# Performance work log

Hardware: AMD Instinct MI355X
Metric: run time of the kernel (lower is better)

Reference implementation:

```python
import jax, jax.numpy as jnp
import numpy as np

INPUT_SIZE = 4
HIDDEN = 2048
OUTPUT_SIZE = 2
NOISE_STD = 0.05
ALPHA = 0.2
RANK = 2
N_SUPPORTS = 2
GDIM = 2 * RANK + INPUT_SIZE  # gaussian_basis_dim default
BATCH = 32
SEQ = 1000


def setup_inputs() -> dict:
    key = jax.random.key(0)
    ks = jax.random.split(key, 8)
    inp = jax.random.normal(ks[0], (BATCH, SEQ, INPUT_SIZE), dtype=jnp.float32)
    noise = jax.random.normal(ks[1], (BATCH, SEQ, HIDDEN), dtype=jnp.float32)
    gaussian_basis = jax.random.normal(ks[2], (GDIM, HIDDEN), dtype=jnp.float32)
    # supports: block indicator masks over hidden units (equal split, weights=None)
    sup = np.zeros((N_SUPPORTS, HIDDEN), dtype=np.float32)
    l = HIDDEN // N_SUPPORTS
    for i in range(N_SUPPORTS):
        sup[i, l * i:l * (i + 1)] = 1.0
    supports = jnp.asarray(sup)
    wi_weights = jax.random.normal(ks[3], (INPUT_SIZE, N_SUPPORTS, GDIM), dtype=jnp.float32)
    m_weights = jax.random.normal(ks[4], (RANK, N_SUPPORTS, GDIM), dtype=jnp.float32) / jnp.sqrt(jnp.float32(HIDDEN))
    n_weights = jax.random.normal(ks[5], (RANK, N_SUPPORTS, GDIM), dtype=jnp.float32) / jnp.sqrt(jnp.float32(HIDDEN))
    wo_weights = jax.random.normal(ks[6], (OUTPUT_SIZE, N_SUPPORTS, GDIM), dtype=jnp.float32) / jnp.float32(HIDDEN)
    wi_biases = jnp.zeros((INPUT_SIZE, N_SUPPORTS), dtype=jnp.float32)
    m_biases = jnp.zeros((RANK, N_SUPPORTS), dtype=jnp.float32)
    n_biases = jnp.zeros((RANK, N_SUPPORTS), dtype=jnp.float32)
    h0_weights = jnp.zeros((N_SUPPORTS, GDIM), dtype=jnp.float32)
    return {
        "input": inp, "noise": noise,
        "wi_weights": wi_weights, "m_weights": m_weights, "n_weights": n_weights,
        "wo_weights": wo_weights, "wi_biases": wi_biases, "m_biases": m_biases,
        "n_biases": n_biases, "h0_weights": h0_weights,
        "gaussian_basis": gaussian_basis, "supports": supports,
    }


def _proxy_params(wi_weights, m_weights, n_weights, wo_weights,
                  wi_biases, m_biases, n_biases, h0_weights,
                  gaussian_basis, supports):
    # (X, S, G) @ (G, H) -> (X, S, H); mask by supports (S, H); sum over S
    def mix(w):
        return jnp.einsum('xsg,gh->xsh', w, gaussian_basis)
    wi = jnp.sum(mix(wi_weights) * supports, axis=1) + wi_biases @ supports      # (I, H)
    m = (jnp.sum(mix(m_weights) * supports, axis=1) + m_biases @ supports).T     # (H, R)
    n = (jnp.sum(mix(n_weights) * supports, axis=1) + n_biases @ supports).T     # (H, R)
    wo = jnp.sum(mix(wo_weights) * supports, axis=1).T                            # (H, O)
    h0 = jnp.sum((h0_weights @ gaussian_basis) * supports, axis=0)                # (H,)
    return wi, m, n, wo, h0


def reference(input, noise, wi_weights, m_weights, n_weights, wo_weights,
              wi_biases, m_biases, n_biases, h0_weights, gaussian_basis, supports):
    wi, m, n, wo, h0 = _proxy_params(wi_weights, m_weights, n_weights, wo_weights,
                                     wi_biases, m_biases, n_biases, h0_weights,
                                     gaussian_basis, supports)
    B = input.shape[0]
    # Precompute external input projection for all steps: (B, T, H)
    xin = jnp.einsum('bti,ih->bth', input, wi)
    h_init = jnp.broadcast_to(h0, (B, h0.shape[0]))
    r_init = jnp.tanh(h_init)

    noise_T = jnp.swapaxes(noise, 0, 1)  # (T, B, H)
    xin_T = jnp.swapaxes(xin, 0, 1)      # (T, B, H)

    def step(carry, xs):
        h, r = carry
        noise_t, xin_t = xs
        h = h + NOISE_STD * noise_t + ALPHA * (-h + (r @ n) @ m.T + xin_t)
        r = jnp.tanh(h)
        return (h, r), r

    _, rs = jax.lax.scan(step, (h_init, r_init), (noise_T, xin_T))  # rs: (T, B, H)
    output = jnp.einsum('tbh,ho->bto', rs, wo)  # (B, T, O)
    return output
```

## Files before the change

### kernel.cpp

```cpp
#include <hip/hip_runtime.h>

#define BATCH 32
#define SEQT 1000
#define INSZ 4
#define HID 2048
#define NOISE_STD 0.05f
#define ALPHA 0.2f
#define ONE_M_ALPHA (1.0f - ALPHA)

#define NTHREADS 512
#define NWAVES 8
#define EPT 4
#define PF 4

typedef float v2f __attribute__((ext_vector_type(2)));

__device__ __forceinline__ v2f pk_fma(v2f a, v2f b, v2f c) {
    v2f d; asm("v_pk_fma_f32 %0, %1, %2, %3" : "=v"(d) : "v"(a), "v"(b), "v"(c)); return d;
}
__device__ __forceinline__ v2f pk_mul(v2f a, v2f b) {
    v2f d; asm("v_pk_mul_f32 %0, %1, %2" : "=v"(d) : "v"(a), "v"(b)); return d;
}
__device__ __forceinline__ v2f pk_add(v2f a, v2f b) {
    v2f d; asm("v_pk_add_f32 %0, %1, %2" : "=v"(d) : "v"(a), "v"(b)); return d;
}
#define C2(v) (v2f{(v), (v)})


__device__ __forceinline__ void tree64_pair(float& a, float& b) {
    asm("s_nop 1\n\t"
        "v_add_f32_dpp %0, %0, %0 row_shr:1 row_mask:0xf bank_mask:0xf bound_ctrl:0\n\t"
        "v_add_f32_dpp %1, %1, %1 row_shr:1 row_mask:0xf bank_mask:0xf bound_ctrl:0\n\t"
        "v_add_f32_dpp %0, %0, %0 row_shr:2 row_mask:0xf bank_mask:0xf bound_ctrl:0\n\t"
        "v_add_f32_dpp %1, %1, %1 row_shr:2 row_mask:0xf bank_mask:0xf bound_ctrl:0\n\t"
        "v_add_f32_dpp %0, %0, %0 row_shr:4 row_mask:0xf bank_mask:0xf bound_ctrl:0\n\t"
        "v_add_f32_dpp %1, %1, %1 row_shr:4 row_mask:0xf bank_mask:0xf bound_ctrl:0\n\t"
        "v_add_f32_dpp %0, %0, %0 row_shr:8 row_mask:0xf bank_mask:0xf bound_ctrl:0\n\t"
        "v_add_f32_dpp %1, %1, %1 row_shr:8 row_mask:0xf bank_mask:0xf bound_ctrl:0\n\t"
        "v_add_f32_dpp %0, %0, %0 row_bcast:15 row_mask:0xf bank_mask:0xf bound_ctrl:0\n\t"
        "v_add_f32_dpp %1, %1, %1 row_bcast:15 row_mask:0xf bank_mask:0xf bound_ctrl:0\n\t"
        "v_add_f32_dpp %0, %0, %0 row_bcast:31 row_mask:0xf bank_mask:0xf bound_ctrl:0\n\t"
        "v_add_f32_dpp %1, %1, %1 row_bcast:31 row_mask:0xf bank_mask:0xf bound_ctrl:0"
        : "+v"(a), "+v"(b));
}

__device__ __forceinline__ void bfly8_pair(float& a, float& b) {
    asm("s_nop 1\n\t"
        "v_add_f32_dpp %0, %0, %0 quad_perm:[1,0,3,2] row_mask:0xf bank_mask:0xf\n\t"
        "v_add_f32_dpp %1, %1, %1 quad_perm:[1,0,3,2] row_mask:0xf bank_mask:0xf\n\t"
        "v_add_f32_dpp %0, %0, %0 quad_perm:[2,3,0,1] row_mask:0xf bank_mask:0xf\n\t"
        "v_add_f32_dpp %1, %1, %1 quad_perm:[2,3,0,1] row_mask:0xf bank_mask:0xf\n\t"
        "v_add_f32_dpp %0, %0, %0 row_half_mirror row_mask:0xf bank_mask:0xf\n\t"
        "v_add_f32_dpp %1, %1, %1 row_half_mirror row_mask:0xf bank_mask:0xf"
        : "+v"(a), "+v"(b));
}

__device__ __forceinline__ v2f pade_tanh(v2f x) {
    const v2f x2  = pk_mul(x, x);
    const v2f num = pk_mul(x, pk_fma(x2, pk_add(x2, C2(105.0f)), C2(945.0f)));
    const v2f den = pk_fma(x2, pk_fma(x2, C2(15.0f), C2(420.0f)), C2(945.0f));
    v2f r;
    r.x = num.x * __builtin_amdgcn_rcpf(den.x);
    r.y = num.y * __builtin_amdgcn_rcpf(den.y);
    r.x = fminf(fmaxf(r.x, -1.0f), 1.0f);
    r.y = fminf(fmaxf(r.y, -1.0f), 1.0f);
    return r;
}

__device__ __forceinline__ float pade_tanh_s(float x) {
    const float x2 = x * x;
    const float num = x * fmaf(x2, x2 + 105.0f, 945.0f);
    const float den = fmaf(x2, fmaf(x2, 15.0f, 420.0f), 945.0f);
    float r = num * __builtin_amdgcn_rcpf(den);
    return fminf(fmaxf(r, -1.0f), 1.0f);
}

#define LDS_BARRIER() __asm__ volatile("s_waitcnt lgkmcnt(0)\ns_barrier" ::: "memory")

__global__ __launch_bounds__(NTHREADS)
void rnn_kernel(const float* __restrict__ input,
                const float* __restrict__ noise,
                const float* __restrict__ wi_w,
                const float* __restrict__ m_w,
                const float* __restrict__ n_w,
                const float* __restrict__ wo_w,
                const float* __restrict__ wi_b,
                const float* __restrict__ m_b,
                const float* __restrict__ n_b,
                const float* __restrict__ h0_w,
                const float* __restrict__ gb,
                const float* __restrict__ sup,
                float* __restrict__ out)
{
    __shared__ __align__(16) float2 sDup[SEQT][4];
    __shared__ float2 sW[2][NWAVES][65];
    __shared__ float2 sO[2][NWAVES][65];

    const int b    = blockIdx.x;
    const int tid  = threadIdx.x;
    const int wave = tid >> 6;
    const int lane = tid & 63;

    const float4* inRow4 = reinterpret_cast<const float4*>(input + (size_t)b * SEQT * INSZ);
    for (int i = tid; i < SEQT; i += NTHREADS) {
        const float4 v = inRow4[i];
        sDup[i][0] = make_float2(v.x, v.x);
        sDup[i][1] = make_float2(v.y, v.y);
        sDup[i][2] = make_float2(v.z, v.z);
        sDup[i][3] = make_float2(v.w, v.w);
    }

    v2f wiA[INSZ][2];
    v2f mA0v[2], mA1v[2], n0v[2], n1v[2], wo0v[2], wo1v[2], hv[2];
    v2f q0 = {0.f, 0.f}, q1 = q0, q2 = q0, q3 = q0;

    #pragma unroll
    for (int e = 0; e < EPT; ++e) {
        const int h = tid * 4 + e;
        const int pi = e >> 1, pc = e & 1;
        float gv[8];
        #pragma unroll
        for (int g = 0; g < 8; ++g) gv[g] = gb[g * HID + h];
        const float s0 = sup[h];
        const float s1 = sup[HID + h];

        auto mix = [&](const float* w) -> float {
            float a0 = 0.f, a1 = 0.f;
            #pragma unroll
            for (int g = 0; g < 8; ++g) { a0 += w[g] * gv[g]; a1 += w[8 + g] * gv[g]; }
            return s0 * a0 + s1 * a1;
        };

        #pragma unroll
        for (int i = 0; i < INSZ; ++i)
            wiA[i][pi][pc] = ALPHA * (mix(wi_w + i * 16) + wi_b[i * 2 + 0] * s0 + wi_b[i * 2 + 1] * s1);
        mA0v[pi][pc] = ALPHA * (mix(m_w)      + m_b[0] * s0 + m_b[1] * s1);
        mA1v[pi][pc] = ALPHA * (mix(m_w + 16) + m_b[2] * s0 + m_b[3] * s1);
        const float n0 = mix(n_w)      + n_b[0] * s0 + n_b[1] * s1;
        const float n1 = mix(n_w + 16) + n_b[2] * s0 + n_b[3] * s1;
        const float w0 = mix(wo_w);
        const float w1 = mix(wo_w + 16);
        n0v[pi][pc] = n0;  n1v[pi][pc] = n1;
        wo0v[pi][pc] = w0; wo1v[pi][pc] = w1;
        {
            float a0 = 0.f, a1 = 0.f;
            #pragma unroll
            for (int g = 0; g < 8; ++g) { a0 += h0_w[g] * gv[g]; a1 += h0_w[8 + g] * gv[g]; }
            const float h0v = s0 * a0 + s1 * a1;
            hv[pi][pc] = h0v;
            const float r = pade_tanh_s(h0v);
            q0[pc] += r * n0;  q1[pc] += r * n1;
            q2[pc] += r * w0;  q3[pc] += r * w1;
        }
    }

    const float4* nP4 = reinterpret_cast<const float4*>(noise + (size_t)b * SEQT * HID);
    const int rowStride = HID / 4;
    float4 nb0 = nP4[0 * rowStride + tid];
    float4 nb1 = nP4[1 * rowStride + tid];
    float4 nb2 = nP4[2 * rowStride + tid];
    float4 nb3 = nP4[3 * rowStride + tid];

    float* outRow = out + (size_t)b * SEQT * 2;

    __syncthreads();
    const float4* dRow = reinterpret_cast<const float4*>(sDup);
    float4 ivA0 = dRow[0], ivB0 = dRow[1];
    float4 ivA1 = dRow[2], ivB1 = dRow[3];
    float4 ivA2 = dRow[4], ivB2 = dRow[5];
    float4 ivA3 = dRow[6], ivB3 = dRow[7];

    const v2f cNS  = C2(NOISE_STD);
    const v2f cOMA = C2(ONE_M_ALPHA);

    auto do_step = [&](int t, int PAR, float4& nbuf, float4& ivAreg, float4& ivBreg) {
        float w0 = q0.x + q0.y;
        float w1 = q1.x + q1.y;
        tree64_pair(w0, w1);
        sW[PAR][wave][lane] = make_float2(w0, w1);

        LDS_BARRIER();

        const float2 prw = sW[PAR][lane & 7][63];
        const float2 pro = sO[PAR ^ 1][lane & 7][63];

        float oz = q2.x + q2.y;
        float ow = q3.x + q3.y;
        tree64_pair(oz, ow);
        sO[PAR][wave][lane] = make_float2(oz, ow);

        const int tpre = (t + PF < SEQT) ? (t + PF) : (SEQT - 1);
        const float4 nv4 = nbuf;
        nbuf = nP4[(size_t)tpre * rowStride + tid];
        const float4 ivA = ivAreg, ivB = ivBreg;
        ivAreg = dRow[2 * tpre];
        ivBreg = dRow[2 * tpre + 1];

        const v2f nlo = {nv4.x, nv4.y}, nhi = {nv4.z, nv4.w};
        const v2f ix = {ivA.x, ivA.y}, iy = {ivA.z, ivA.w};
        const v2f iz = {ivB.x, ivB.y}, iw = {ivB.z, ivB.w};
        v2f acc0 = pk_mul(wiA[0][0], ix);
        v2f acc1 = pk_mul(wiA[0][1], ix);
        acc0 = pk_fma(wiA[1][0], iy, acc0);  acc1 = pk_fma(wiA[1][1], iy, acc1);
        acc0 = pk_fma(wiA[2][0], iz, acc0);  acc1 = pk_fma(wiA[2][1], iz, acc1);
        acc0 = pk_fma(wiA[3][0], iw, acc0);  acc1 = pk_fma(wiA[3][1], iw, acc1);
        acc0 = pk_fma(nlo, cNS, acc0);       acc1 = pk_fma(nhi, cNS, acc1);
        acc0 = pk_fma(hv[0], cOMA, acc0);    acc1 = pk_fma(hv[1], cOMA, acc1);

        float y0 = prw.x, y1 = prw.y;
        bfly8_pair(y0, y1);

        float o0 = pro.x, o1 = pro.y;
        bfly8_pair(o0, o1);
        if (t >= 2 && tid == ((t & 7) << 6))
            *reinterpret_cast<float2*>(outRow + (t - 2) * 2) = make_float2(o0, o1);

        const v2f y0p = {y0, y0}, y1p = {y1, y1};
        v2f h2a = pk_fma(mA1v[0], y1p, acc0);
        v2f h2b = pk_fma(mA1v[1], y1p, acc1);
        h2a = pk_fma(mA0v[0], y0p, h2a);
        h2b = pk_fma(mA0v[1], y0p, h2b);
        hv[0] = h2a; hv[1] = h2b;
        const v2f r2a = pade_tanh(h2a);
        const v2f r2b = pade_tanh(h2b);
        q0 = pk_fma(r2b, n0v[1],  pk_mul(r2a, n0v[0]));
        q1 = pk_fma(r2b, n1v[1],  pk_mul(r2a, n1v[0]));
        q2 = pk_fma(r2b, wo0v[1], pk_mul(r2a, wo0v[0]));
        q3 = pk_fma(r2b, wo1v[1], pk_mul(r2a, wo1v[0]));
    };

    for (int t = 0; t < SEQT; t += PF) {
        do_step(t,     0, nb0, ivA0, ivB0);
        do_step(t + 1, 1, nb1, ivA1, ivB1);
        do_step(t + 2, 0, nb2, ivA2, ivB2);
        do_step(t + 3, 1, nb3, ivA3, ivB3);
    }

    {
        float a9 = q2.x + q2.y;
        float b9 = q3.x + q3.y;
        tree64_pair(a9, b9);
        sW[0][wave][lane] = make_float2(a9, b9);
        LDS_BARRIER();
        const float2 pr9 = sW[0][lane & 7][63];
        const float2 pr8 = sO[1][lane & 7][63];
        float x9 = pr9.x, y9 = pr9.y;
        float x8 = pr8.x, y8 = pr8.y;
        bfly8_pair(x9, y9);
        bfly8_pair(x8, y8);
        if (tid == 0) {
            *reinterpret_cast<float2*>(outRow + 998 * 2) = make_float2(x8, y8);
            *reinterpret_cast<float2*>(outRow + 999 * 2) = make_float2(x9, y9);
        }
    }
}

extern "C" void kernel_launch(void* const* d_in, const int* in_sizes, int n_in,
                              void* d_out, int out_size, void* d_ws, size_t ws_size,
                              hipStream_t stream) {
    const float* input = (const float*)d_in[0];
    const float* noise = (const float*)d_in[1];
    const float* wi_w  = (const float*)d_in[2];
    const float* m_w   = (const float*)d_in[3];
    const float* n_w   = (const float*)d_in[4];
    const float* wo_w  = (const float*)d_in[5];
    const float* wi_b  = (const float*)d_in[6];
    const float* m_b   = (const float*)d_in[7];
    const float* n_b   = (const float*)d_in[8];
    const float* h0_w  = (const float*)d_in[9];
    const float* gb    = (const float*)d_in[10];
    const float* sup   = (const float*)d_in[11];
    float* out = (float*)d_out;

    rnn_kernel<<<dim3(BATCH), dim3(NTHREADS), 0, stream>>>(
        input, noise, wi_w, m_w, n_w, wo_w, wi_b, m_b, n_b, h0_w, gb, sup, out);
}
```

Measured before the change: 830.4 us.

## Halve block to 4 waves with 8 elements per thread and merge reductions

Shrinks each block from 512 to 256 threads, so each thread owns 8 hidden units and the cross-wave exchange covers 4 waves instead of 8. The recurrence reduction and the output reduction are merged into one four-value DPP tree and one float4 LDS slot, removing the separate output exchange array. This cuts barrier cost and the per-step cross-wave combine latency on the serial critical path. In exchange each thread does twice the per-step elementwise work and needs more registers.

```diff
diff --git a/kernel.cpp b/kernel.cpp
--- a/kernel.cpp
+++ b/kernel.cpp
@@ -8,9 +8,10 @@
 #define ALPHA 0.2f
 #define ONE_M_ALPHA (1.0f - ALPHA)
 
-#define NTHREADS 512
-#define NWAVES 8
-#define EPT 4
+#define NTHREADS 256
+#define NWAVES 4
+#define EPT 8
+#define NPAIR 4
 #define PF 4
 
 typedef float v2f __attribute__((ext_vector_type(2)));
@@ -26,6 +27,34 @@
 }
 #define C2(v) (v2f{(v), (v)})
 
+__device__ __forceinline__ void tree64_quad(float& a, float& b, float& c, float& d) {
+    asm("s_nop 1\n\t"
+        "v_add_f32_dpp %0, %0, %0 row_shr:1 row_mask:0xf bank_mask:0xf bound_ctrl:0\n\t"
+        "v_add_f32_dpp %1, %1, %1 row_shr:1 row_mask:0xf bank_mask:0xf bound_ctrl:0\n\t"
+        "v_add_f32_dpp %2, %2, %2 row_shr:1 row_mask:0xf bank_mask:0xf bound_ctrl:0\n\t"
+        "v_add_f32_dpp %3, %3, %3 row_shr:1 row_mask:0xf bank_mask:0xf bound_ctrl:0\n\t"
+        "v_add_f32_dpp %0, %0, %0 row_shr:2 row_mask:0xf bank_mask:0xf bound_ctrl:0\n\t"
+        "v_add_f32_dpp %1, %1, %1 row_shr:2 row_mask:0xf bank_mask:0xf bound_ctrl:0\n\t"
+        "v_add_f32_dpp %2, %2, %2 row_shr:2 row_mask:0xf bank_mask:0xf bound_ctrl:0\n\t"
+        "v_add_f32_dpp %3, %3, %3 row_shr:2 row_mask:0xf bank_mask:0xf bound_ctrl:0\n\t"
+        "v_add_f32_dpp %0, %0, %0 row_shr:4 row_mask:0xf bank_mask:0xf bound_ctrl:0\n\t"
+        "v_add_f32_dpp %1, %1, %1 row_shr:4 row_mask:0xf bank_mask:0xf bound_ctrl:0\n\t"
+        "v_add_f32_dpp %2, %2, %2 row_shr:4 row_mask:0xf bank_mask:0xf bound_ctrl:0\n\t"
+        "v_add_f32_dpp %3, %3, %3 row_shr:4 row_mask:0xf bank_mask:0xf bound_ctrl:0\n\t"
+        "v_add_f32_dpp %0, %0, %0 row_shr:8 row_mask:0xf bank_mask:0xf bound_ctrl:0\n\t"
+        "v_add_f32_dpp %1, %1, %1 row_shr:8 row_mask:0xf bank_mask:0xf bound_ctrl:0\n\t"
+        "v_add_f32_dpp %2, %2, %2 row_shr:8 row_mask:0xf bank_mask:0xf bound_ctrl:0\n\t"
+        "v_add_f32_dpp %3, %3, %3 row_shr:8 row_mask:0xf bank_mask:0xf bound_ctrl:0\n\t"
+        "v_add_f32_dpp %0, %0, %0 row_bcast:15 row_mask:0xf bank_mask:0xf bound_ctrl:0\n\t"
+        "v_add_f32_dpp %1, %1, %1 row_bcast:15 row_mask:0xf bank_mask:0xf bound_ctrl:0\n\t"
+        "v_add_f32_dpp %2, %2, %2 row_bcast:15 row_mask:0xf bank_mask:0xf bound_ctrl:0\n\t"
+        "v_add_f32_dpp %3, %3, %3 row_bcast:15 row_mask:0xf bank_mask:0xf bound_ctrl:0\n\t"
+        "v_add_f32_dpp %0, %0, %0 row_bcast:31 row_mask:0xf bank_mask:0xf bound_ctrl:0\n\t"
+        "v_add_f32_dpp %1, %1, %1 row_bcast:31 row_mask:0xf bank_mask:0xf bound_ctrl:0\n\t"
+        "v_add_f32_dpp %2, %2, %2 row_bcast:31 row_mask:0xf bank_mask:0xf bound_ctrl:0\n\t"
+        "v_add_f32_dpp %3, %3, %3 row_bcast:31 row_mask:0xf bank_mask:0xf bound_ctrl:0"
+        : "+v"(a), "+v"(b), "+v"(c), "+v"(d));
+}
 
 __device__ __forceinline__ void tree64_pair(float& a, float& b) {
     asm("s_nop 1\n\t"
@@ -44,14 +73,25 @@
         : "+v"(a), "+v"(b));
 }
 
-__device__ __forceinline__ void bfly8_pair(float& a, float& b) {
+__device__ __forceinline__ void bfly4_quad(float& a, float& b, float& c, float& d) {
+    asm("s_nop 1\n\t"
+        "v_add_f32_dpp %0, %0, %0 quad_perm:[1,0,3,2] row_mask:0xf bank_mask:0xf\n\t"
+        "v_add_f32_dpp %1, %1, %1 quad_perm:[1,0,3,2] row_mask:0xf bank_mask:0xf\n\t"
+        "v_add_f32_dpp %2, %2, %2 quad_perm:[1,0,3,2] row_mask:0xf bank_mask:0xf\n\t"
+        "v_add_f32_dpp %3, %3, %3 quad_perm:[1,0,3,2] row_mask:0xf bank_mask:0xf\n\t"
+        "v_add_f32_dpp %0, %0, %0 quad_perm:[2,3,0,1] row_mask:0xf bank_mask:0xf\n\t"
+        "v_add_f32_dpp %1, %1, %1 quad_perm:[2,3,0,1] row_mask:0xf bank_mask:0xf\n\t"
+        "v_add_f32_dpp %2, %2, %2 quad_perm:[2,3,0,1] row_mask:0xf bank_mask:0xf\n\t"
+        "v_add_f32_dpp %3, %3, %3 quad_perm:[2,3,0,1] row_mask:0xf bank_mask:0xf"
+        : "+v"(a), "+v"(b), "+v"(c), "+v"(d));
+}
+
+__device__ __forceinline__ void bfly4_pair(float& a, float& b) {
     asm("s_nop 1\n\t"
         "v_add_f32_dpp %0, %0, %0 quad_perm:[1,0,3,2] row_mask:0xf bank_mask:0xf\n\t"
         "v_add_f32_dpp %1, %1, %1 quad_perm:[1,0,3,2] row_mask:0xf bank_mask:0xf\n\t"
         "v_add_f32_dpp %0, %0, %0 quad_perm:[2,3,0,1] row_mask:0xf bank_mask:0xf\n\t"
-        "v_add_f32_dpp %1, %1, %1 quad_perm:[2,3,0,1] row_mask:0xf bank_mask:0xf\n\t"
-        "v_add_f32_dpp %0, %0, %0 row_half_mirror row_mask:0xf bank_mask:0xf\n\t"
-        "v_add_f32_dpp %1, %1, %1 row_half_mirror row_mask:0xf bank_mask:0xf"
+        "v_add_f32_dpp %1, %1, %1 quad_perm:[2,3,0,1] row_mask:0xf bank_mask:0xf"
         : "+v"(a), "+v"(b));
 }
 
@@ -93,8 +133,7 @@
                 float* __restrict__ out)
 {
     __shared__ __align__(16) float2 sDup[SEQT][4];
-    __shared__ float2 sW[2][NWAVES][65];
-    __shared__ float2 sO[2][NWAVES][65];
+    __shared__ __align__(16) float4 sW4[2][NWAVES][65];
 
     const int b    = blockIdx.x;
     const int tid  = threadIdx.x;
@@ -110,13 +149,13 @@
         sDup[i][3] = make_float2(v.w, v.w);
     }
 
-    v2f wiA[INSZ][2];
-    v2f mA0v[2], mA1v[2], n0v[2], n1v[2], wo0v[2], wo1v[2], hv[2];
+    v2f wiA[INSZ][NPAIR];
+    v2f mA0v[NPAIR], mA1v[NPAIR], n0v[NPAIR], n1v[NPAIR], wo0v[NPAIR], wo1v[NPAIR], hv[NPAIR];
     v2f q0 = {0.f, 0.f}, q1 = q0, q2 = q0, q3 = q0;
 
     #pragma unroll
     for (int e = 0; e < EPT; ++e) {
-        const int h = tid * 4 + e;
+        const int h = tid * EPT + e;
         const int pi = e >> 1, pc = e & 1;
         float gv[8];
         #pragma unroll
@@ -156,10 +195,11 @@
 
     const float4* nP4 = reinterpret_cast<const float4*>(noise + (size_t)b * SEQT * HID);
     const int rowStride = HID / 4;
-    float4 nb0 = nP4[0 * rowStride + tid];
-    float4 nb1 = nP4[1 * rowStride + tid];
-    float4 nb2 = nP4[2 * rowStride + tid];
-    float4 nb3 = nP4[3 * rowStride + tid];
+    const int nbase = tid * 2;
+    float4 na0 = nP4[0 * rowStride + nbase], nb0 = nP4[0 * rowStride + nbase + 1];
+    float4 na1 = nP4[1 * rowStride + nbase], nb1 = nP4[1 * rowStride + nbase + 1];
+    float4 na2 = nP4[2 * rowStride + nbase], nb2 = nP4[2 * rowStride + nbase + 1];
+    float4 na3 = nP4[3 * rowStride + nbase], nb3 = nP4[3 * rowStride + nbase + 1];
 
     float* outRow = out + (size_t)b * SEQT * 2;
 
@@ -173,85 +213,85 @@
     const v2f cNS  = C2(NOISE_STD);
     const v2f cOMA = C2(ONE_M_ALPHA);
 
-    auto do_step = [&](int t, int PAR, float4& nbuf, float4& ivAreg, float4& ivBreg) {
+    auto do_step = [&](int t, int PAR, float4& nA, float4& nB, float4& ivAreg, float4& ivBreg) {
         float w0 = q0.x + q0.y;
         float w1 = q1.x + q1.y;
-        tree64_pair(w0, w1);
-        sW[PAR][wave][lane] = make_float2(w0, w1);
-
-        LDS_BARRIER();
-
-        const float2 prw = sW[PAR][lane & 7][63];
-        const float2 pro = sO[PAR ^ 1][lane & 7][63];
-
         float oz = q2.x + q2.y;
         float ow = q3.x + q3.y;
-        tree64_pair(oz, ow);
-        sO[PAR][wave][lane] = make_float2(oz, ow);
+        tree64_quad(w0, w1, oz, ow);
+        sW4[PAR][wave][lane] = make_float4(w0, w1, oz, ow);
+
+        LDS_BARRIER();
+
+        const float4 pr = sW4[PAR][lane & 3][63];
 
         const int tpre = (t + PF < SEQT) ? (t + PF) : (SEQT - 1);
-        const float4 nv4 = nbuf;
-        nbuf = nP4[(size_t)tpre * rowStride + tid];
+        const float4 nv4a = nA, nv4b = nB;
+        nA = nP4[(size_t)tpre * rowStride + nbase];
+        nB = nP4[(size_t)tpre * rowStride + nbase + 1];
         const float4 ivA = ivAreg, ivB = ivBreg;
         ivAreg = dRow[2 * tpre];
         ivBreg = dRow[2 * tpre + 1];
 
-        const v2f nlo = {nv4.x, nv4.y}, nhi = {nv4.z, nv4.w};
         const v2f ix = {ivA.x, ivA.y}, iy = {ivA.z, ivA.w};
         const v2f iz = {ivB.x, ivB.y}, iw = {ivB.z, ivB.w};
-        v2f acc0 = pk_mul(wiA[0][0], ix);
-        v2f acc1 = pk_mul(wiA[0][1], ix);
-        acc0 = pk_fma(wiA[1][0], iy, acc0);  acc1 = pk_fma(wiA[1][1], iy, acc1);
-        acc0 = pk_fma(wiA[2][0], iz, acc0);  acc1 = pk_fma(wiA[2][1], iz, acc1);
-        acc0 = pk_fma(wiA[3][0], iw, acc0);  acc1 = pk_fma(wiA[3][1], iw, acc1);
-        acc0 = pk_fma(nlo, cNS, acc0);       acc1 = pk_fma(nhi, cNS, acc1);
-        acc0 = pk_fma(hv[0], cOMA, acc0);    acc1 = pk_fma(hv[1], cOMA, acc1);
-
-        float y0 = prw.x, y1 = prw.y;
-        bfly8_pair(y0, y1);
-
-        float o0 = pro.x, o1 = pro.y;
-        bfly8_pair(o0, o1);
-        if (t >= 2 && tid == ((t & 7) << 6))
-            *reinterpret_cast<float2*>(outRow + (t - 2) * 2) = make_float2(o0, o1);
+        const v2f nn[NPAIR] = { {nv4a.x, nv4a.y}, {nv4a.z, nv4a.w},
+                                {nv4b.x, nv4b.y}, {nv4b.z, nv4b.w} };
+        v2f acc[NPAIR];
+        #pragma unroll
+        for (int p = 0; p < NPAIR; ++p) {
+            acc[p] = pk_mul(wiA[0][p], ix);
+            acc[p] = pk_fma(wiA[1][p], iy, acc[p]);
+            acc[p] = pk_fma(wiA[2][p], iz, acc[p]);
+            acc[p] = pk_fma(wiA[3][p], iw, acc[p]);
+            acc[p] = pk_fma(nn[p], cNS, acc[p]);
+            acc[p] = pk_fma(hv[p], cOMA, acc[p]);
+        }
+
+        float y0 = pr.x, y1 = pr.y, o0 = pr.z, o1 = pr.w;
+        bfly4_quad(y0, y1, o0, o1);
+
+        if (t >= 1 && tid == ((t & 3) << 6))
+            *reinterpret_cast<float2*>(outRow + (t - 1) * 2) = make_float2(o0, o1);
 
         const v2f y0p = {y0, y0}, y1p = {y1, y1};
-        v2f h2a = pk_fma(mA1v[0], y1p, acc0);
-        v2f h2b = pk_fma(mA1v[1], y1p, acc1);
-        h2a = pk_fma(mA0v[0], y0p, h2a);
-        h2b = pk_fma(mA0v[1], y0p, h2b);
-        hv[0] = h2a; hv[1] = h2b;
-        const v2f r2a = pade_tanh(h2a);
-        const v2f r2b = pade_tanh(h2b);
-        q0 = pk_fma(r2b, n0v[1],  pk_mul(r2a, n0v[0]));
-        q1 = pk_fma(r2b, n1v[1],  pk_mul(r2a, n1v[0]));
-        q2 = pk_fma(r2b, wo0v[1], pk_mul(r2a, wo0v[0]));
-        q3 = pk_fma(r2b, wo1v[1], pk_mul(r2a, wo1v[0]));
+        v2f r[NPAIR];
+        #pragma unroll
+        for (int p = 0; p < NPAIR; ++p) {
+            v2f h2 = pk_fma(mA1v[p], y1p, acc[p]);
+            h2 = pk_fma(mA0v[p], y0p, h2);
+            hv[p] = h2;
+            r[p] = pade_tanh(h2);
+        }
+        q0 = pk_mul(r[0], n0v[0]);  q1 = pk_mul(r[0], n1v[0]);
+        q2 = pk_mul(r[0], wo0v[0]); q3 = pk_mul(r[0], wo1v[0]);
+        #pragma unroll
+        for (int p = 1; p < NPAIR; ++p) {
+            q0 = pk_fma(r[p], n0v[p],  q0);
+            q1 = pk_fma(r[p], n1v[p],  q1);
+            q2 = pk_fma(r[p], wo0v[p], q2);
+            q3 = pk_fma(r[p], wo1v[p], q3);
+        }
     };
 
     for (int t = 0; t < SEQT; t += PF) {
-        do_step(t,     0, nb0, ivA0, ivB0);
-        do_step(t + 1, 1, nb1, ivA1, ivB1);
-        do_step(t + 2, 0, nb2, ivA2, ivB2);
-        do_step(t + 3, 1, nb3, ivA3, ivB3);
+        do_step(t,     0, na0, nb0, ivA0, ivB0);
+        do_step(t + 1, 1, na1, nb1, ivA1, ivB1);
+        do_step(t + 2, 0, na2, nb2, ivA2, ivB2);
+        do_step(t + 3, 1, na3, nb3, ivA3, ivB3);
     }
 
     {
         float a9 = q2.x + q2.y;
         float b9 = q3.x + q3.y;
         tree64_pair(a9, b9);
-        sW[0][wave][lane] = make_float2(a9, b9);
+        sW4[0][wave][lane] = make_float4(a9, b9, 0.f, 0.f);
         LDS_BARRIER();
-        const float2 pr9 = sW[0][lane & 7][63];
-        const float2 pr8 = sO[1][lane & 7][63];
-        float x9 = pr9.x, y9 = pr9.y;
-        float x8 = pr8.x, y8 = pr8.y;
-        bfly8_pair(x9, y9);
-        bfly8_pair(x8, y8);
-        if (tid == 0) {
-            *reinterpret_cast<float2*>(outRow + 998 * 2) = make_float2(x8, y8);
+        const float4 pr = sW4[0][lane & 3][63];
+        float x9 = pr.x, y9 = pr.y;
+        bfly4_pair(x9, y9);
+        if (tid == 0)
             *reinterpret_cast<float2*>(outRow + 999 * 2) = make_float2(x9, y9);
-        }
     }
 }
 
```

Result: faster. 800.7 us (-3.6%).
